# Optimization experiments

Hardware: AMD Instinct MI355X
Metric: run time of the kernel (lower is better)

Reference implementation:

```python
import jax, jax.numpy as jnp
import numpy as np

C = 256
C8 = C // 8
B, H, W = 4, 64, 64


def setup_inputs() -> dict:
    key = jax.random.key(0)
    ks = jax.random.split(key, 10)
    s = lambda fan_in: 1.0 / np.sqrt(fan_in)
    return {
        "x": jax.random.normal(ks[0], (B, C, H, W), dtype=jnp.float32),
        "conv_w": jax.random.normal(ks[1], (C8, C), dtype=jnp.float32) * s(C),
        "conv_b": jax.random.normal(ks[2], (C8,), dtype=jnp.float32) * 0.01,
        "q_w": jax.random.normal(ks[3], (C8, C8), dtype=jnp.float32) * s(C8),
        "q_b": jax.random.normal(ks[4], (C8,), dtype=jnp.float32) * 0.01,
        "k_w": jax.random.normal(ks[5], (C8, C8), dtype=jnp.float32) * s(C8),
        "k_b": jax.random.normal(ks[6], (C8,), dtype=jnp.float32) * 0.01,
        "v_w": jax.random.normal(ks[7], (C, C8), dtype=jnp.float32) * s(C8),
        "v_b": jax.random.normal(ks[8], (C,), dtype=jnp.float32) * 0.01,
        "gamma": jax.random.normal(ks[9], (1,), dtype=jnp.float32) * 0.1,
    }


def reference(x, conv_w, conv_b, q_w, q_b, k_w, k_b, v_w, v_b, gamma):
    b, c, h, w = x.shape
    hw = h * w
    # 1x1 convs are channel-mixing matmuls over flattened spatial dims
    xf = x.reshape(b, c, hw)                                   # [B, C, HW]
    proj = jnp.einsum('dc,bcn->bdn', conv_w, xf) + conv_b[None, :, None]   # [B, C8, HW]
    q = jnp.einsum('ed,bdn->bne', q_w, proj) + q_b[None, None, :]          # [B, HW, C8]
    k = jnp.einsum('ed,bdn->ben', k_w, proj) + k_b[None, :, None]          # [B, C8, HW]
    v = jnp.einsum('cd,bdn->bcn', v_w, proj) + v_b[None, :, None]          # [B, C, HW]
    attn = jax.nn.softmax(jnp.einsum('bne,bem->bnm', q, k), axis=-1)       # [B, HW, HW]
    out = jnp.einsum('bcm,bnm->bcn', v, attn)                              # [B, C, HW]
    out = out.reshape(b, c, h, w)
    return gamma[0] * out + x
```

## Files before the change

kernel.cpp:

```cpp
#include <hip/hip_runtime.h>
#include <hip/hip_bf16.h>
#include <stdint.h>

#define B_   4
#define C_   256
#define C8_  32
#define HW_  4096
#define ROWS_ 320
#define MS_  4
#define L2E  1.4426950408889634f

typedef __attribute__((ext_vector_type(8)))  short  short8;
typedef __attribute__((ext_vector_type(8)))  ushort us8;
typedef __attribute__((ext_vector_type(2)))  float  f32x2;
typedef __attribute__((ext_vector_type(16))) float  f32x16;

#define WT_OFF    0
#define BALL_OFF  (256*320*4)
#define Q_OFF     (BALL_OFF + 1280)
#define KT_OFF    (Q_OFF  + B_*HW_*C8_*2)
#define V_OFF     (KT_OFF + B_*HW_*C8_*2)
#define PACC_OFF  (V_OFF  + B_*C_*HW_*2)
#define LPART_OFF (PACC_OFF + (size_t)MS_*B_*C_*HW_*2)

__device__ __forceinline__ ushort f2bf(float f) {
    union { float f; uint32_t u; } v; v.f = f;
    uint32_t u = v.u;
    uint32_t r = u + 0x7fffu + ((u >> 16) & 1u);
    return (ushort)(r >> 16);
}
__device__ __forceinline__ uint32_t pktr(float lo, float hi) {
    union { float f; uint32_t u; } a, b; a.f = lo; b.f = hi;
    return __builtin_amdgcn_perm(b.u, a.u, 0x07060302u);
}
__device__ __forceinline__ uint32_t fexp2_pk(float s0, float s1, f32x2& e01) {
    f32x2 s = {s0, s1};
    f32x2 y = __builtin_elementwise_fma(s, (f32x2)(8388608.0f),
                                        (f32x2)(1064992506.0f));
    y = __builtin_elementwise_max(y, (f32x2)(0.0f));
    union { int i; float f; } c0, c1;
    c0.i = (int)y.x;  c1.i = (int)y.y;
    e01.x = c0.f;  e01.y = c1.f;
    return __builtin_amdgcn_perm((uint32_t)c1.i, (uint32_t)c0.i, 0x07060302u);
}

__global__ __launch_bounds__(256) void k_setup(
    const float* __restrict__ conv_w, const float* __restrict__ conv_b,
    const float* __restrict__ q_w, const float* __restrict__ q_b,
    const float* __restrict__ k_w, const float* __restrict__ k_b,
    const float* __restrict__ v_w, const float* __restrict__ v_b,
    ushort* __restrict__ wbf, float* __restrict__ ball)
{
    int r = blockIdx.x;
    int c = threadIdx.x;
    const float* wrow;
    float bias;
    if (r < 32)       { wrow = q_w + r*32;      bias = q_b[r];      }
    else if (r < 64)  { wrow = k_w + (r-32)*32; bias = k_b[r-32];   }
    else              { wrow = v_w + (r-64)*32; bias = v_b[r-64];   }
    float acc = 0.f;
    #pragma unroll
    for (int d = 0; d < 32; ++d) acc += wrow[d] * conv_w[d*C_ + c];
    float scale = (r < 32) ? L2E : 1.0f;
    int lanew = (r & 31) + 32*((c >> 3) & 1);
    int fidx  = (c >> 4)*10 + (r >> 5);
    wbf[fidx*512 + lanew*8 + (c & 7)] = f2bf(acc * scale);
    if (c == 0) {
        float bb = bias;
        #pragma unroll
        for (int d = 0; d < 32; ++d) bb += wrow[d] * conv_b[d];
        ball[r] = bb * scale;
    }
}

__global__ __launch_bounds__(320) void k_qkv(
    const float* __restrict__ x, const ushort* __restrict__ wbf,
    const float* __restrict__ ball,
    ushort* __restrict__ qg, ushort* __restrict__ ktg, ushort* __restrict__ vg)
{
    __shared__ ushort tr[5][32*40];

    int blk = blockIdx.x;
    int b  = blk >> 7;
    int nt = blk & 127;
    int n0 = nt * 32;
    int t = threadIdx.x;
    int w = t >> 6, lane = t & 63;
    int l31 = lane & 31, h = lane >> 5;

    f32x16 acc[2];
    acc[0] = (f32x16)(0.f);
    acc[1] = (f32x16)(0.f);

    const float* xb = x + (size_t)b*C_*HW_ + n0 + l31;

    #pragma unroll 2
    for (int kc = 0; kc < 16; ++kc) {
        short8 a0 = *(const short8*)(wbf + (kc*10 + w*2    )*512 + lane*8);
        short8 a1 = *(const short8*)(wbf + (kc*10 + w*2 + 1)*512 + lane*8);
        const float* xc = xb + (size_t)(kc*16 + h*8)*HW_;
        union { uint32_t d[4]; short8 s8; } bf;
        #pragma unroll
        for (int j2 = 0; j2 < 4; ++j2) {
            float f0 = xc[(size_t)(2*j2    )*HW_];
            float f1 = xc[(size_t)(2*j2 + 1)*HW_];
            bf.d[j2] = pktr(f0, f1);
        }
        acc[0] = __builtin_amdgcn_mfma_f32_32x32x16_bf16(a0, bf.s8, acc[0], 0, 0, 0);
        acc[1] = __builtin_amdgcn_mfma_f32_32x32x16_bf16(a1, bf.s8, acc[1], 0, 0, 0);
    }

    #pragma unroll
    for (int mi = 0; mi < 2; ++mi) {
        int rowb = w*64 + mi*32;
        bool isQK = (rowb < 64);
        #pragma unroll
        for (int r = 0; r < 16; ++r) {
            int roff = (r & 3) + 8*(r >> 2) + 4*h;
            ushort bv = f2bf(acc[mi][r] + ball[rowb + roff]);
            int ad = isQK ? (l31*40 + roff) : (roff*40 + l31);
            tr[w][ad] = bv;
        }
        __syncthreads();
        #pragma unroll
        for (int f = 0; f < 2; ++f) {
            us8 frag = *(const us8*)(&tr[w][l31*40 + f*16 + h*8]);
            if (isQK) {
                ushort* dstb = (rowb == 0) ? qg : ktg;
                size_t ad = ((size_t)((b*128 + nt)*2 + f) << 9) + lane*8;
                *(us8*)(dstb + ad) = frag;
            } else {
                int cblk = (rowb - 64) >> 5;
                int mb = nt*2 + f;
                size_t ad = ((size_t)((b*8 + cblk)*256 + mb) << 9) + lane*8;
                *(us8*)(vg + ad) = frag;
            }
        }
        __syncthreads();
    }
}

__global__ __launch_bounds__(512, 4) void k_attn(
    const ushort* __restrict__ qg, const ushort* __restrict__ ktg,
    const ushort* __restrict__ vg,
    ushort* __restrict__ pacc, float* __restrict__ lpart)
{
    __shared__ ushort v_lds[2][16*512];
    __shared__ ushort kt_lds[2][4*512];

    int blk = blockIdx.x;
    int ms = blk & 3;
    int cs = (blk >> 2) & 1;
    int qb = (blk >> 3) & 15;
    int b  = blk >> 7;
    int t = threadIdx.x;
    int w = t >> 6, lane = t & 63;
    int l31 = lane & 31, h = lane >> 5;
    int mbase = ms*1024;

    short8 qf[2];
    #pragma unroll
    for (int ks = 0; ks < 2; ++ks)
        qf[ks] = *(const short8*)(qg
            + ((size_t)((b*128 + qb*8 + w)*2 + ks) << 9) + lane*8);

    f32x16 acc[4];
    #pragma unroll
    for (int j = 0; j < 4; ++j) acc[j] = (f32x16)(0.f);
    f32x2 lacc0 = {0.f, 0.f};
    f32x2 lacc1 = {0.f, 0.f};

    #define STAGE(buf, m0)                                                          \
    {                                                                               \
        _Pragma("unroll")                                                           \
        for (int ff = 0; ff < 2; ++ff) {                                            \
            int f = w*2 + ff;                                                       \
            int cfr = f >> 2, mf = f & 3;                                           \
            const ushort* src = vg + ((size_t)((b*8 + cs*4 + cfr)*256               \
                                 + ((m0) >> 4) + mf) << 9) + lane*8;                \
            __builtin_amdgcn_global_load_lds(                                       \
                (const __attribute__((address_space(1))) uint32_t*)src,             \
                (__attribute__((address_space(3))) uint32_t*)&v_lds[buf][f*512],    \
                16, 0, 0);                                                          \
        }                                                                           \
        if (w < 4) {                                                                \
            const ushort* src = ktg + ((size_t)((b*128 + ((m0) >> 5) + (w >> 1))*2  \
                                 + (w & 1)) << 9) + lane*8;                         \
            __builtin_amdgcn_global_load_lds(                                       \
                (const __attribute__((address_space(1))) uint32_t*)src,             \
                (__attribute__((address_space(3))) uint32_t*)&kt_lds[buf][w*512],   \
                16, 0, 0);                                                          \
        }                                                                           \
    }

    #define PMERGE(uu, lo8, hi8)                                                    \
    {                                                                               \
        union { uint32_t d[4]; short8 s8; } fe_, fo_;                               \
        auto r02 = __builtin_amdgcn_permlane32_swap((int)uu[0], (int)uu[2], false, false); \
        auto r13 = __builtin_amdgcn_permlane32_swap((int)uu[1], (int)uu[3], false, false); \
        auto r46 = __builtin_amdgcn_permlane32_swap((int)uu[4], (int)uu[6], false, false); \
        auto r57 = __builtin_amdgcn_permlane32_swap((int)uu[5], (int)uu[7], false, false); \
        fe_.d[0] = (uint32_t)r02[0];  fe_.d[1] = (uint32_t)r13[0];                  \
        fe_.d[2] = (uint32_t)r02[1];  fe_.d[3] = (uint32_t)r13[1];                  \
        fo_.d[0] = (uint32_t)r46[0];  fo_.d[1] = (uint32_t)r57[0];                  \
        fo_.d[2] = (uint32_t)r46[1];  fo_.d[3] = (uint32_t)r57[1];                  \
        lo8 = fe_.s8;  hi8 = fo_.s8;                                               \
    }

    STAGE(0, mbase)
    __syncthreads();

    int buf = 0;
    for (int it = 0; it < 16; ++it) {
        if (it + 1 < 16) STAGE(buf ^ 1, mbase + (it+1)*64)

        short8 kt0a = *(const short8*)(&kt_lds[buf][0*512 + lane*8]);
        short8 kt1a = *(const short8*)(&kt_lds[buf][1*512 + lane*8]);
        f32x16 s_a = (f32x16)(0.f);
        __builtin_amdgcn_s_setprio(1);
        s_a = __builtin_amdgcn_mfma_f32_32x32x16_bf16(kt0a, qf[0], s_a, 0, 0, 0);
        s_a = __builtin_amdgcn_mfma_f32_32x32x16_bf16(kt1a, qf[1], s_a, 0, 0, 0);
        __builtin_amdgcn_s_setprio(0);

        uint32_t ua[8];
        #pragma unroll
        for (int i = 0; i < 8; ++i) {
            f32x2 e01;
            ua[i] = fexp2_pk(s_a[2*i], s_a[2*i+1], e01);
            if (i & 1) lacc1 += e01; else lacc0 += e01;
        }
        short8 pfa0, pfa1;
        PMERGE(ua, pfa0, pfa1)

        short8 kt0b = *(const short8*)(&kt_lds[buf][2*512 + lane*8]);
        short8 kt1b = *(const short8*)(&kt_lds[buf][3*512 + lane*8]);
        f32x16 s_b = (f32x16)(0.f);
        s_b = __builtin_amdgcn_mfma_f32_32x32x16_bf16(kt0b, qf[0], s_b, 0, 0, 0);
        s_b = __builtin_amdgcn_mfma_f32_32x32x16_bf16(kt1b, qf[1], s_b, 0, 0, 0);

        uint32_t ub[8];
        #pragma unroll
        for (int i = 0; i < 8; ++i) {
            f32x2 e01;
            ub[i] = fexp2_pk(s_b[2*i], s_b[2*i+1], e01);
            if (i & 1) lacc1 += e01; else lacc0 += e01;
        }
        #pragma unroll
        for (int msub = 0; msub < 2; ++msub) {
            short8 pfm = msub ? pfa1 : pfa0;
            int ks16 = msub;
            #pragma unroll
            for (int cfr = 0; cfr < 4; ++cfr) {
                short8 vf = *(const short8*)(&v_lds[buf][(cfr*4 + ks16)*512 + lane*8]);
                acc[cfr] = __builtin_amdgcn_mfma_f32_32x32x16_bf16(vf, pfm, acc[cfr], 0, 0, 0);
            }
        }
        short8 pfb0, pfb1;
        PMERGE(ub, pfb0, pfb1)

        __builtin_amdgcn_s_setprio(1);
        #pragma unroll
        for (int msub = 0; msub < 2; ++msub) {
            short8 pfm = msub ? pfb1 : pfb0;
            int ks16 = 2 + msub;
            #pragma unroll
            for (int cfr = 0; cfr < 4; ++cfr) {
                short8 vf = *(const short8*)(&v_lds[buf][(cfr*4 + ks16)*512 + lane*8]);
                acc[cfr] = __builtin_amdgcn_mfma_f32_32x32x16_bf16(vf, pfm, acc[cfr], 0, 0, 0);
            }
        }
        __builtin_amdgcn_s_setprio(0);

        __syncthreads();
        buf ^= 1;
    }

    f32x2 lacc = lacc0 + lacc1;
    float lsum = lacc.x + lacc.y;
    {
        union { float f; int i; } cv; cv.f = lsum;
        cv.i = __shfl_xor(cv.i, 32);
        lsum += cv.f;
    }
    if (cs == 0 && h == 0)
        lpart[(size_t)(ms*B_ + b)*HW_ + qb*256 + w*32 + l31] = lsum;

    int blkl = ((ms*B_ + b)*16 + qb)*2 + cs;
    #pragma unroll
    for (int cfr = 0; cfr < 4; ++cfr) {
        union { uint32_t d[8]; us8 hlf[2]; } pk;
        #pragma unroll
        for (int i = 0; i < 8; ++i)
            pk.d[i] = pktr(acc[cfr][2*i], acc[cfr][2*i+1]);
        ushort* dst = pacc + ((size_t)(blkl*32 + w*4 + cfr) << 10);
        *(us8*)(dst + lane*8)       = pk.hlf[0];
        *(us8*)(dst + 512 + lane*8) = pk.hlf[1];
    }
    #undef STAGE
    #undef PMERGE
}

__global__ __launch_bounds__(256) void k_comb(
    const ushort* __restrict__ pacc, const float* __restrict__ lpart,
    const float* __restrict__ x, const float* __restrict__ gamma_p,
    float* __restrict__ out)
{
    __shared__ float lds_acc[128*36];

    int blk = blockIdx.x;
    int w  = blk & 7;
    int cs = (blk >> 3) & 1;
    int qb = (blk >> 4) & 15;
    int b  = blk >> 8;
    int t = threadIdx.x;

    int l31 = t & 31;
    int h   = (t >> 5) & 1;
    int cfr = (t >> 6) & 3;
    int q = qb*256 + w*32 + l31;
    int lanef = h*32 + l31;

    float sum[16];
    #pragma unroll
    for (int k = 0; k < 16; ++k) sum[k] = 0.f;
    float lt = 0.f;

    #pragma unroll
    for (int ms = 0; ms < MS_; ++ms) {
        int blkl = ((ms*B_ + b)*16 + qb)*2 + cs;
        const ushort* pp = pacc + ((size_t)(blkl*32 + w*4 + cfr) << 10) + lanef*8;
        us8 a0 = *(const us8*)pp;
        us8 a1 = *(const us8*)(pp + 512);
        #pragma unroll
        for (int k = 0; k < 8; ++k) {
            union { uint32_t u; float f; } cv;
            cv.u = ((uint32_t)a0[k]) << 16;  sum[k]   += cv.f;
            cv.u = ((uint32_t)a1[k]) << 16;  sum[k+8] += cv.f;
        }
        lt += lpart[(size_t)(ms*B_ + b)*HW_ + q];
    }

    float rl = gamma_p[0] / lt;
    #pragma unroll
    for (int k = 0; k < 16; ++k) {
        int c = cfr*32 + (k & 3) + 8*(k >> 2) + 4*h;
        lds_acc[c*36 + l31] = sum[k]*rl;
    }
    __syncthreads();

    const float* xb = x + ((size_t)(b*C_ + cs*128))*HW_ + qb*256 + w*32;
    float* ob = out + ((size_t)(b*C_ + cs*128))*HW_ + qb*256 + w*32;
    #pragma unroll
    for (int i = 0; i < 4; ++i) {
        int s = t + i*256;
        int c = s >> 3, qg = s & 7;
        float4 a = *(const float4*)(&lds_acc[c*36 + qg*4]);
        size_t off = (size_t)c*HW_ + qg*4;
        float4 xv = *(const float4*)(xb + off);
        a.x += xv.x; a.y += xv.y; a.z += xv.z; a.w += xv.w;
        *(float4*)(ob + off) = a;
    }
}

extern "C" void kernel_launch(void* const* d_in, const int* in_sizes, int n_in,
                              void* d_out, int out_size, void* d_ws, size_t ws_size,
                              hipStream_t stream)
{
    const float* x      = (const float*)d_in[0];
    const float* conv_w = (const float*)d_in[1];
    const float* conv_b = (const float*)d_in[2];
    const float* q_w    = (const float*)d_in[3];
    const float* q_b    = (const float*)d_in[4];
    const float* k_w    = (const float*)d_in[5];
    const float* k_b    = (const float*)d_in[6];
    const float* v_w    = (const float*)d_in[7];
    const float* v_b    = (const float*)d_in[8];
    const float* gamma  = (const float*)d_in[9];
    float* out = (float*)d_out;

    char* ws = (char*)d_ws;
    ushort* wbf   = (ushort*)(ws + WT_OFF);
    float*  ball  = (float*)(ws + BALL_OFF);
    ushort* qg    = (ushort*)(ws + Q_OFF);
    ushort* ktg   = (ushort*)(ws + KT_OFF);
    ushort* vg    = (ushort*)(ws + V_OFF);
    ushort* pacc  = (ushort*)(ws + PACC_OFF);
    float*  lpart = (float*)(ws + LPART_OFF);

    k_setup<<<ROWS_, 256, 0, stream>>>(conv_w, conv_b, q_w, q_b, k_w, k_b,
                                       v_w, v_b, wbf, ball);
    k_qkv<<<B_*128, 320, 0, stream>>>(x, wbf, ball, qg, ktg, vg);
    k_attn<<<512, 512, 0, stream>>>(qg, ktg, vg, pacc, lpart);
    k_comb<<<1024, 256, 0, stream>>>(pacc, lpart, x, gamma, out);
}
```

Before: 152.9 us.

## Fuse combine step into attention kernel via last-block atomic counter

Removes the separate k_comb launch. Each attention block bumps a per-(batch, query-block, channel-split) atomic counter after writing its partial accumulators and row sums. The last of the four m-split blocks to arrive reduces the partials, applies gamma and the softmax normalisation, and adds the residual x. The intent is to save a kernel launch and let the partials be read back while still cache-resident. The cost is a memset of the counters, extra fences, and a serial combine tail that only 128 blocks execute, each looping over four query sub-tiles.

Result: slower. 190.6 us (+24.7%).

```diff
diff --git a/kernel.cpp b/kernel.cpp
--- a/kernel.cpp
+++ b/kernel.cpp
@@ -22,6 +22,7 @@
 #define V_OFF     (KT_OFF + B_*HW_*C8_*2)
 #define PACC_OFF  (V_OFF  + B_*C_*HW_*2)
 #define LPART_OFF (PACC_OFF + (size_t)MS_*B_*C_*HW_*2)
+#define CNT_OFF   (LPART_OFF + (size_t)MS_*B_*HW_*4)
 
 __device__ __forceinline__ ushort f2bf(float f) {
     union { float f; uint32_t u; } v; v.f = f;
@@ -143,10 +144,14 @@
 __global__ __launch_bounds__(512, 4) void k_attn(
     const ushort* __restrict__ qg, const ushort* __restrict__ ktg,
     const ushort* __restrict__ vg,
-    ushort* __restrict__ pacc, float* __restrict__ lpart)
+    ushort* __restrict__ pacc, float* __restrict__ lpart,
+    const float* __restrict__ x, const float* __restrict__ gamma_p,
+    float* __restrict__ out, uint32_t* __restrict__ cnt)
 {
-    __shared__ ushort v_lds[2][16*512];
-    __shared__ ushort kt_lds[2][4*512];
+    __shared__ __align__(16) char smem[40960];
+    __shared__ int comb_flag;
+    ushort* v_lds  = (ushort*)smem;
+    ushort* kt_lds = (ushort*)(smem + 32768);
 
     int blk = blockIdx.x;
     int ms = blk & 3;
@@ -170,41 +175,43 @@
     f32x2 lacc0 = {0.f, 0.f};
     f32x2 lacc1 = {0.f, 0.f};
 
-    #define STAGE(buf, m0)                                                          \
-    {                                                                               \
-        _Pragma("unroll")                                                           \
-        for (int ff = 0; ff < 2; ++ff) {                                            \
-            int f = w*2 + ff;                                                       \
-            int cfr = f >> 2, mf = f & 3;                                           \
-            const ushort* src = vg + ((size_t)((b*8 + cs*4 + cfr)*256               \
-                                 + ((m0) >> 4) + mf) << 9) + lane*8;                \
-            __builtin_amdgcn_global_load_lds(                                       \
-                (const __attribute__((address_space(1))) uint32_t*)src,             \
-                (__attribute__((address_space(3))) uint32_t*)&v_lds[buf][f*512],    \
-                16, 0, 0);                                                          \
-        }                                                                           \
-        if (w < 4) {                                                                \
-            const ushort* src = ktg + ((size_t)((b*128 + ((m0) >> 5) + (w >> 1))*2  \
-                                 + (w & 1)) << 9) + lane*8;                         \
-            __builtin_amdgcn_global_load_lds(                                       \
-                (const __attribute__((address_space(1))) uint32_t*)src,             \
-                (__attribute__((address_space(3))) uint32_t*)&kt_lds[buf][w*512],   \
-                16, 0, 0);                                                          \
-        }                                                                           \
-    }
-
-    #define PMERGE(uu, lo8, hi8)                                                    \
-    {                                                                               \
-        union { uint32_t d[4]; short8 s8; } fe_, fo_;                               \
+    #define STAGE(bi, m0)                                                          \
+    {                                                                              \
+        _Pragma("unroll")                                                          \
+        for (int ff = 0; ff < 2; ++ff) {                                           \
+            int f = w*2 + ff;                                                      \
+            int cfr = f >> 2, mf = f & 3;                                          \
+            const ushort* src = vg + ((size_t)((b*8 + cs*4 + cfr)*256              \
+                                 + ((m0) >> 4) + mf) << 9) + lane*8;               \
+            __builtin_amdgcn_global_load_lds(                                      \
+                (const __attribute__((address_space(1))) uint32_t*)src,            \
+                (__attribute__((address_space(3))) uint32_t*)                      \
+                    &v_lds[(bi)*8192 + f*512],                                     \
+                16, 0, 0);                                                         \
+        }                                                                          \
+        if (w < 4) {                                                               \
+            const ushort* src = ktg + ((size_t)((b*128 + ((m0) >> 5) + (w >> 1))*2 \
+                                 + (w & 1)) << 9) + lane*8;                        \
+            __builtin_amdgcn_global_load_lds(                                      \
+                (const __attribute__((address_space(1))) uint32_t*)src,            \
+                (__attribute__((address_space(3))) uint32_t*)                      \
+                    &kt_lds[(bi)*2048 + w*512],                                    \
+                16, 0, 0);                                                         \
+        }                                                                          \
+    }
+
+    #define PMERGE(uu, lo8, hi8)                                                   \
+    {                                                                              \
+        union { uint32_t d[4]; short8 s8; } fe_, fo_;                              \
         auto r02 = __builtin_amdgcn_permlane32_swap((int)uu[0], (int)uu[2], false, false); \
         auto r13 = __builtin_amdgcn_permlane32_swap((int)uu[1], (int)uu[3], false, false); \
         auto r46 = __builtin_amdgcn_permlane32_swap((int)uu[4], (int)uu[6], false, false); \
         auto r57 = __builtin_amdgcn_permlane32_swap((int)uu[5], (int)uu[7], false, false); \
-        fe_.d[0] = (uint32_t)r02[0];  fe_.d[1] = (uint32_t)r13[0];                  \
-        fe_.d[2] = (uint32_t)r02[1];  fe_.d[3] = (uint32_t)r13[1];                  \
-        fo_.d[0] = (uint32_t)r46[0];  fo_.d[1] = (uint32_t)r57[0];                  \
-        fo_.d[2] = (uint32_t)r46[1];  fo_.d[3] = (uint32_t)r57[1];                  \
-        lo8 = fe_.s8;  hi8 = fo_.s8;                                               \
+        fe_.d[0] = (uint32_t)r02[0];  fe_.d[1] = (uint32_t)r13[0];                 \
+        fe_.d[2] = (uint32_t)r02[1];  fe_.d[3] = (uint32_t)r13[1];                 \
+        fo_.d[0] = (uint32_t)r46[0];  fo_.d[1] = (uint32_t)r57[0];                 \
+        fo_.d[2] = (uint32_t)r46[1];  fo_.d[3] = (uint32_t)r57[1];                 \
+        lo8 = fe_.s8;  hi8 = fo_.s8;                                              \
     }
 
     STAGE(0, mbase)
@@ -214,8 +221,11 @@
     for (int it = 0; it < 16; ++it) {
         if (it + 1 < 16) STAGE(buf ^ 1, mbase + (it+1)*64)
 
-        short8 kt0a = *(const short8*)(&kt_lds[buf][0*512 + lane*8]);
-        short8 kt1a = *(const short8*)(&kt_lds[buf][1*512 + lane*8]);
+        const ushort* vbuf = &v_lds[buf*8192];
+        const ushort* kbuf = &kt_lds[buf*2048];
+
+        short8 kt0a = *(const short8*)(kbuf + 0*512 + lane*8);
+        short8 kt1a = *(const short8*)(kbuf + 1*512 + lane*8);
         f32x16 s_a = (f32x16)(0.f);
         __builtin_amdgcn_s_setprio(1);
         s_a = __builtin_amdgcn_mfma_f32_32x32x16_bf16(kt0a, qf[0], s_a, 0, 0, 0);
@@ -232,8 +242,8 @@
         short8 pfa0, pfa1;
         PMERGE(ua, pfa0, pfa1)
 
-        short8 kt0b = *(const short8*)(&kt_lds[buf][2*512 + lane*8]);
-        short8 kt1b = *(const short8*)(&kt_lds[buf][3*512 + lane*8]);
+        short8 kt0b = *(const short8*)(kbuf + 2*512 + lane*8);
+        short8 kt1b = *(const short8*)(kbuf + 3*512 + lane*8);
         f32x16 s_b = (f32x16)(0.f);
         s_b = __builtin_amdgcn_mfma_f32_32x32x16_bf16(kt0b, qf[0], s_b, 0, 0, 0);
         s_b = __builtin_amdgcn_mfma_f32_32x32x16_bf16(kt1b, qf[1], s_b, 0, 0, 0);
@@ -251,7 +261,7 @@
             int ks16 = msub;
             #pragma unroll
             for (int cfr = 0; cfr < 4; ++cfr) {
-                short8 vf = *(const short8*)(&v_lds[buf][(cfr*4 + ks16)*512 + lane*8]);
+                short8 vf = *(const short8*)(vbuf + (cfr*4 + ks16)*512 + lane*8);
                 acc[cfr] = __builtin_amdgcn_mfma_f32_32x32x16_bf16(vf, pfm, acc[cfr], 0, 0, 0);
             }
         }
@@ -265,7 +275,7 @@
             int ks16 = 2 + msub;
             #pragma unroll
             for (int cfr = 0; cfr < 4; ++cfr) {
-                short8 vf = *(const short8*)(&v_lds[buf][(cfr*4 + ks16)*512 + lane*8]);
+                short8 vf = *(const short8*)(vbuf + (cfr*4 + ks16)*512 + lane*8);
                 acc[cfr] = __builtin_amdgcn_mfma_f32_32x32x16_bf16(vf, pfm, acc[cfr], 0, 0, 0);
             }
         }
@@ -282,7 +292,7 @@
         cv.i = __shfl_xor(cv.i, 32);
         lsum += cv.f;
     }
-    if (cs == 0 && h == 0)
+    if (h == 0)
         lpart[(size_t)(ms*B_ + b)*HW_ + qb*256 + w*32 + l31] = lsum;
 
     int blkl = ((ms*B_ + b)*16 + qb)*2 + cs;
@@ -296,70 +306,78 @@
         *(us8*)(dst + lane*8)       = pk.hlf[0];
         *(us8*)(dst + 512 + lane*8) = pk.hlf[1];
     }
+
+    __syncthreads();
+    if (t == 0) {
+        __threadfence();
+        uint32_t old = __hip_atomic_fetch_add(&cnt[(b*16 + qb)*2 + cs], 1u,
+                           __ATOMIC_ACQ_REL, __HIP_MEMORY_SCOPE_AGENT);
+        comb_flag = (old == MS_ - 1u) ? 1 : 0;
+        if (comb_flag) __threadfence();
+    }
+    __syncthreads();
+
+    if (comb_flag) {
+        int half = t >> 8;
+        int tl = t & 255;
+        int l31c = tl & 31;
+        int h3   = (tl >> 5) & 1;
+        int cfr3 = (tl >> 6) & 3;
+        int lanef = h3*32 + l31c;
+        float* lds_acc = (float*)(smem + half*18432);
+        float gmv = gamma_p[0];
+
+        #pragma unroll 1
+        for (int wq = 0; wq < 4; ++wq) {
+            int w3 = wq*2 + half;
+            int q = qb*256 + w3*32 + l31c;
+
+            float sum[16];
+            #pragma unroll
+            for (int k = 0; k < 16; ++k) sum[k] = 0.f;
+            float lt = 0.f;
+
+            #pragma unroll
+            for (int msx = 0; msx < MS_; ++msx) {
+                int bl2 = ((msx*B_ + b)*16 + qb)*2 + cs;
+                const ushort* pp = pacc
+                    + ((size_t)(bl2*32 + w3*4 + cfr3) << 10) + lanef*8;
+                us8 a0 = *(const us8*)pp;
+                us8 a1 = *(const us8*)(pp + 512);
+                #pragma unroll
+                for (int k = 0; k < 8; ++k) {
+                    union { uint32_t u; float f; } cv;
+                    cv.u = ((uint32_t)a0[k]) << 16;  sum[k]   += cv.f;
+                    cv.u = ((uint32_t)a1[k]) << 16;  sum[k+8] += cv.f;
+                }
+                lt += lpart[(size_t)(msx*B_ + b)*HW_ + q];
+            }
+
+            float rl = gmv / lt;
+            #pragma unroll
+            for (int k = 0; k < 16; ++k) {
+                int c = cfr3*32 + (k & 3) + 8*(k >> 2) + 4*h3;
+                lds_acc[c*36 + l31c] = sum[k]*rl;
+            }
+            __syncthreads();
+
+            const float* xb2 = x + ((size_t)(b*C_ + cs*128))*HW_ + qb*256 + w3*32;
+            float* ob = out + ((size_t)(b*C_ + cs*128))*HW_ + qb*256 + w3*32;
+            #pragma unroll
+            for (int i = 0; i < 4; ++i) {
+                int s = tl + i*256;
+                int c = s >> 3, qg2 = s & 7;
+                float4 a = *(const float4*)(&lds_acc[c*36 + qg2*4]);
+                size_t off = (size_t)c*HW_ + qg2*4;
+                float4 xv = *(const float4*)(xb2 + off);
+                a.x += xv.x; a.y += xv.y; a.z += xv.z; a.w += xv.w;
+                *(float4*)(ob + off) = a;
+            }
+            __syncthreads();
+        }
+    }
     #undef STAGE
     #undef PMERGE
-}
-
-__global__ __launch_bounds__(256) void k_comb(
-    const ushort* __restrict__ pacc, const float* __restrict__ lpart,
-    const float* __restrict__ x, const float* __restrict__ gamma_p,
-    float* __restrict__ out)
-{
-    __shared__ float lds_acc[128*36];
-
-    int blk = blockIdx.x;
-    int w  = blk & 7;
-    int cs = (blk >> 3) & 1;
-    int qb = (blk >> 4) & 15;
-    int b  = blk >> 8;
-    int t = threadIdx.x;
-
-    int l31 = t & 31;
-    int h   = (t >> 5) & 1;
-    int cfr = (t >> 6) & 3;
-    int q = qb*256 + w*32 + l31;
-    int lanef = h*32 + l31;
-
-    float sum[16];
-    #pragma unroll
-    for (int k = 0; k < 16; ++k) sum[k] = 0.f;
-    float lt = 0.f;
-
-    #pragma unroll
-    for (int ms = 0; ms < MS_; ++ms) {
-        int blkl = ((ms*B_ + b)*16 + qb)*2 + cs;
-        const ushort* pp = pacc + ((size_t)(blkl*32 + w*4 + cfr) << 10) + lanef*8;
-        us8 a0 = *(const us8*)pp;
-        us8 a1 = *(const us8*)(pp + 512);
-        #pragma unroll
-        for (int k = 0; k < 8; ++k) {
-            union { uint32_t u; float f; } cv;
-            cv.u = ((uint32_t)a0[k]) << 16;  sum[k]   += cv.f;
-            cv.u = ((uint32_t)a1[k]) << 16;  sum[k+8] += cv.f;
-        }
-        lt += lpart[(size_t)(ms*B_ + b)*HW_ + q];
-    }
-
-    float rl = gamma_p[0] / lt;
-    #pragma unroll
-    for (int k = 0; k < 16; ++k) {
-        int c = cfr*32 + (k & 3) + 8*(k >> 2) + 4*h;
-        lds_acc[c*36 + l31] = sum[k]*rl;
-    }
-    __syncthreads();
-
-    const float* xb = x + ((size_t)(b*C_ + cs*128))*HW_ + qb*256 + w*32;
-    float* ob = out + ((size_t)(b*C_ + cs*128))*HW_ + qb*256 + w*32;
-    #pragma unroll
-    for (int i = 0; i < 4; ++i) {
-        int s = t + i*256;
-        int c = s >> 3, qg = s & 7;
-        float4 a = *(const float4*)(&lds_acc[c*36 + qg*4]);
-        size_t off = (size_t)c*HW_ + qg*4;
-        float4 xv = *(const float4*)(xb + off);
-        a.x += xv.x; a.y += xv.y; a.z += xv.z; a.w += xv.w;
-        *(float4*)(ob + off) = a;
-    }
 }
 
 extern "C" void kernel_launch(void* const* d_in, const int* in_sizes, int n_in,
@@ -386,10 +404,13 @@
     ushort* vg    = (ushort*)(ws + V_OFF);
     ushort* pacc  = (ushort*)(ws + PACC_OFF);
     float*  lpart = (float*)(ws + LPART_OFF);
+    uint32_t* cnt = (uint32_t*)(ws + CNT_OFF);
+
+    hipMemsetAsync(cnt, 0, 512, stream);
 
     k_setup<<<ROWS_, 256, 0, stream>>>(conv_w, conv_b, q_w, q_b, k_w, k_b,
                                        v_w, v_b, wbf, ball);
     k_qkv<<<B_*128, 320, 0, stream>>>(x, wbf, ball, qg, ktg, vg);
-    k_attn<<<512, 512, 0, stream>>>(qg, ktg, vg, pacc, lpart);
-    k_comb<<<1024, 256, 0, stream>>>(pacc, lpart, x, gamma, out);
-}
+    k_attn<<<512, 512, 0, stream>>>(qg, ktg, vg, pacc, lpart,
+                                    x, gamma, out, cnt);
+}
```
